# Performance work log

Measured on AMD Instinct MI355X. Metric: run time of the kernel, lower is better.

Reference implementation:

```python
import jax, jax.numpy as jnp
import numpy as np
from jax import lax

N, IC, OC, K, SDIM, H, W = 16, 512, 512, 3, 512, 32, 32
PAD, STRIDE, LR = 1, 1, 1.0
WEIGHT_SCALER = 1.0 / np.sqrt(IC * K * K) * LR   # equalized-lr conv scale
FC_SCALER = 1.0 / np.sqrt(SDIM) * LR             # equalized-lr fc scale


def setup_inputs() -> dict:
    key = jax.random.key(0)
    k1, k2, k3 = jax.random.split(key, 3)
    x = jax.random.normal(k1, (N, IC, H, W), dtype=jnp.float32)
    style = jax.random.normal(k2, (N, SDIM), dtype=jnp.float32)
    weight = jax.random.normal(k3, (OC, IC, K, K), dtype=jnp.float32)  # std = 1/lr = 1
    fc_weight = jax.random.normal(jax.random.fold_in(key, 10), (IC, SDIM), dtype=jnp.float32)
    fc_bias = jnp.zeros((IC,), dtype=jnp.float32)
    return {"x": x, "style": style, "weight": weight,
            "fc_weight": fc_weight, "fc_bias": fc_bias}


def reference(x, style, weight, fc_weight, fc_bias):
    # EqualizedFullyConnect + AddChannelwiseBias, then +1 -> modulation rates [N, iC]
    mod = jnp.einsum('ns,cs->nc', style, fc_weight) * FC_SCALER + fc_bias * LR + 1.0
    # modulated per-sample weight [N, oC, iC, kH, kW]
    w = WEIGHT_SCALER * weight[None] * mod[:, None, :, None, None]
    # demodulate: rsqrt of sum of squares over (iC, kH, kW)
    demod = lax.rsqrt(jnp.sum(w * w, axis=(2, 3, 4)) + 1e-8)  # [N, oC]
    w = w * demod[:, :, None, None, None]
    # grouped conv with groups=N == per-sample conv: vmap over batch
    def conv1(xi, wi):
        # xi: [iC,H,W], wi: [oC,iC,kH,kW]
        return lax.conv_general_dilated(
            xi[None], wi, window_strides=(STRIDE, STRIDE),
            padding=((PAD, PAD), (PAD, PAD)),
            dimension_numbers=('NCHW', 'OIHW', 'NCHW'))[0]
    out = jax.vmap(conv1)(x, w)  # [N, oC, H, W]
    return out
```

## Files before the change

kernel.cpp:

```cpp
#include <hip/hip_runtime.h>
#include <hip/hip_bf16.h>

#define N_    16
#define IC_   512
#define OC_   512
#define SDIM_ 512
#define H_    32
#define W_    32
#define HW_   1024

#define FC_SCALER 0.04419417382415922f
#define WS_       0.014731391274719738f
#define WS2_      (1.0f/4608.0f)

typedef __attribute__((__ext_vector_type__(8)))  __bf16 bf16x8;
typedef __attribute__((__ext_vector_type__(16))) float  f32x16;
typedef __attribute__((__ext_vector_type__(4)))  int    i32x4;

__device__ __forceinline__ unsigned short f2bf(float f) {
    unsigned int u = __builtin_bit_cast(unsigned int, f);
    unsigned int r = (u + 0x7FFFu + ((u >> 16) & 1u)) >> 16;
    return (unsigned short)r;
}

__global__ void k_mod(const float* __restrict__ style, const float* __restrict__ fcw,
                      const float* __restrict__ fcb, float* __restrict__ mod) {
    int gid = blockIdx.x * blockDim.x + threadIdx.x;
    int wid = gid >> 6, lane = gid & 63;
    if (wid >= N_ * IC_) return;
    int n = wid >> 9, c = wid & 511;
    const float4* sp = (const float4*)(style + n * SDIM_);
    const float4* wp = (const float4*)(fcw + (size_t)c * SDIM_);
    float acc = 0.f;
    for (int i = lane; i < SDIM_ / 4; i += 64) {
        float4 a = sp[i], b = wp[i];
        acc += a.x*b.x + a.y*b.y + a.z*b.z + a.w*b.w;
    }
#pragma unroll
    for (int off = 32; off; off >>= 1) acc += __shfl_xor(acc, off);
    if (lane == 0) mod[wid] = acc * FC_SCALER + fcb[c] + 1.0f;
}

__global__ void k_wprep(const float* __restrict__ w, unsigned short* __restrict__ wt,
                        float* __restrict__ wsq) {
    int tid = blockIdx.x * blockDim.x + threadIdx.x;
    int oc = tid >> 9, ic = tid & 511;
    float s = 0.f;
#pragma unroll
    for (int t = 0; t < 9; t++) {
        float v = w[(size_t)tid * 9 + t];
        s += v * v;
        wt[((size_t)(t * OC_ + oc)) * IC_ + ic] = f2bf(v);
    }
    wsq[tid] = s;
}

__global__ void k_demod(const float* __restrict__ mod, const float* __restrict__ wsq,
                        float* __restrict__ demod_ws) {
    int gid = blockIdx.x * blockDim.x + threadIdx.x;
    int wid = gid >> 6, lane = gid & 63;
    if (wid >= N_ * OC_) return;
    int n = wid >> 9, oc = wid & 511;
    const float4* mp = (const float4*)(mod + n * IC_);
    const float4* qp = (const float4*)(wsq + (size_t)oc * IC_);
    float acc = 0.f;
    for (int i = lane; i < IC_ / 4; i += 64) {
        float4 m = mp[i], q = qp[i];
        acc += m.x*m.x*q.x + m.y*m.y*q.y + m.z*m.z*q.z + m.w*m.w*q.w;
    }
#pragma unroll
    for (int off = 32; off; off >>= 1) acc += __shfl_xor(acc, off);
    if (lane == 0) {
        float s = WS2_ * acc + 1e-8f;
        demod_ws[wid] = WS_ / sqrtf(s);
    }
}

__global__ void k_premod(const float* __restrict__ x, const float* __restrict__ mod,
                         unsigned short* __restrict__ xm) {
    __shared__ __align__(16) unsigned short t_lds[64][80];
    int bx = blockIdx.x;
    int n = bx >> 7, hwt = (bx >> 3) & 15, ict = bx & 7;
    int hw0 = hwt * 64, ic0 = ict * 64;
    int tid = threadIdx.x, lane = tid & 63, ty = tid >> 6;
#pragma unroll
    for (int jj = 0; jj < 16; jj++) {
        int icl = ty * 16 + jj;
        float v = x[(size_t)(n * IC_ + ic0 + icl) * HW_ + hw0 + lane]
                  * mod[n * IC_ + ic0 + icl];
        t_lds[lane][icl] = f2bf(v);
    }
    __syncthreads();
#pragma unroll
    for (int rep = 0; rep < 2; rep++) {
        int hwl = rep * 32 + (tid >> 3);
        int icl8 = (tid & 7) * 8;
        i32x4 v = *(const i32x4*)&t_lds[hwl][icl8];
        *(i32x4*)(xm + ((size_t)(n * HW_ + hw0 + hwl) * IC_ + ic0 + icl8)) = v;
    }
}

#define BLK_OC 128
__global__ __launch_bounds__(256, 2)
void k_conv(const unsigned short* __restrict__ xm, const unsigned short* __restrict__ wt,
            const float* __restrict__ demod_ws, float* __restrict__ out) {
    __shared__ __align__(16) unsigned short xt[6 * 34 * 64];
    __shared__ __align__(16) unsigned short wbuf[2][128 * 64];
    __shared__ float s_demod[128];

    int bx = blockIdx.x;
    int n = bx >> 5, octile = (bx >> 3) & 3, sptile = bx & 7;
    int oc0 = octile * BLK_OC, y0 = sptile * 4;
    int tid = threadIdx.x, lane = tid & 63, wid = tid >> 6;
    int wr = wid >> 1, wc = wid & 1;

    if (tid < 128) s_demod[tid] = demod_ws[n * OC_ + oc0 + tid];

    f32x16 acc[2][2] = {};

    const unsigned short* xbase = xm + (size_t)n * HW_ * IC_;

#pragma unroll 1
    for (int icc = 0; icc < IC_ / 64; icc++) {
        int ic0 = icc * 64;
        for (int idx = tid; idx < 6 * 34 * 8; idx += 256) {
            int rc = idx >> 3, icl8 = (idx & 7) * 8;
            int rr = rc / 34, cp = rc - rr * 34;
            int yy = y0 - 1 + rr, xx = cp - 1;
            i32x4 v = {};
            if ((unsigned)yy < 32u && (unsigned)xx < 32u)
                v = *(const i32x4*)(xbase + ((size_t)(yy * W_ + xx) * IC_ + ic0 + icl8));
            int a = (rc * 128 + icl8 * 2) ^ ((rc & 7) << 4);
            *(i32x4*)((char*)xt + a) = v;
        }
        {
            const unsigned short* wsrc = wt + (size_t)oc0 * IC_ + ic0;
#pragma unroll
            for (int k = 0; k < 4; k++) {
                int c = tid + k * 256;
                int ocl = c >> 3, icl8 = (c & 7) * 8;
                i32x4 v = *(const i32x4*)(wsrc + (size_t)ocl * IC_ + icl8);
                int a = (ocl * 128 + icl8 * 2) ^ ((ocl & 7) << 4);
                *(i32x4*)((char*)wbuf[0] + a) = v;
            }
        }
        __syncthreads();

#pragma unroll
        for (int t = 0; t < 9; t++) {
            i32x4 wreg[4];
            if (t < 8) {
                const unsigned short* wsrc =
                    wt + ((size_t)((t + 1) * OC_ + oc0)) * IC_ + ic0;
#pragma unroll
                for (int k = 0; k < 4; k++) {
                    int c = tid + k * 256;
                    int ocl = c >> 3, icl8 = (c & 7) * 8;
                    wreg[k] = *(const i32x4*)(wsrc + (size_t)ocl * IC_ + icl8);
                }
            }
            int dy = t / 3, dx = t % 3;
            const unsigned short* wb = wbuf[t & 1];
#pragma unroll
            for (int kk = 0; kk < 4; kk++) {
                int koff = kk * 16 + (lane >> 5) * 8;
                bf16x8 af[2], bfr[2];
#pragma unroll
                for (int fo = 0; fo < 2; fo++) {
                    int ocl = wr * 64 + fo * 32 + (lane & 31);
                    int a = (ocl * 128 + koff * 2) ^ ((ocl & 7) << 4);
                    af[fo] = *(const bf16x8*)((const char*)wb + a);
                }
#pragma unroll
                for (int fs = 0; fs < 2; fs++) {
                    int rr = wc * 2 + fs + dy;
                    int cp = (lane & 31) + dx;
                    int rc = rr * 34 + cp;
                    int a = (rc * 128 + koff * 2) ^ ((rc & 7) << 4);
                    bfr[fs] = *(const bf16x8*)((const char*)xt + a);
                }
#pragma unroll
                for (int fo = 0; fo < 2; fo++)
#pragma unroll
                    for (int fs = 0; fs < 2; fs++)
                        acc[fo][fs] = __builtin_amdgcn_mfma_f32_32x32x16_bf16(
                            af[fo], bfr[fs], acc[fo][fs], 0, 0, 0);
            }
            if (t < 8) {
#pragma unroll
                for (int k = 0; k < 4; k++) {
                    int c = tid + k * 256;
                    int ocl = c >> 3, icl8 = (c & 7) * 8;
                    int a = (ocl * 128 + icl8 * 2) ^ ((ocl & 7) << 4);
                    *(i32x4*)((char*)wbuf[(t + 1) & 1] + a) = wreg[k];
                }
            }
            __syncthreads();
        }
    }

    int xcol = lane & 31;
#pragma unroll
    for (int fo = 0; fo < 2; fo++) {
#pragma unroll
        for (int fs = 0; fs < 2; fs++) {
            int y = y0 + wc * 2 + fs;
#pragma unroll
            for (int r = 0; r < 16; r++) {
                int row = (r & 3) + 8 * (r >> 2) + 4 * (lane >> 5);
                int ocl = wr * 64 + fo * 32 + row;
                float v = acc[fo][fs][r] * s_demod[ocl];
                out[((size_t)(n * OC_ + oc0 + ocl) * H_ + y) * W_ + xcol] = v;
            }
        }
    }
}

extern "C" void kernel_launch(void* const* d_in, const int* in_sizes, int n_in,
                              void* d_out, int out_size, void* d_ws, size_t ws_size,
                              hipStream_t stream) {
    const float* x      = (const float*)d_in[0];
    const float* style  = (const float*)d_in[1];
    const float* weight = (const float*)d_in[2];
    const float* fcw    = (const float*)d_in[3];
    const float* fcb    = (const float*)d_in[4];
    float* out = (float*)d_out;

    char* ws = (char*)d_ws;
    float*          mod   = (float*)ws;
    float*          demod = (float*)(ws + 32768);
    float*          wsq   = (float*)(ws + 65536);
    unsigned short* wtb   = (unsigned short*)(ws + 65536 + 1048576);
    unsigned short* xmb   = (unsigned short*)(ws + 65536 + 1048576 + 4718592);

    k_mod   <<<2048, 256, 0, stream>>>(style, fcw, fcb, mod);
    k_wprep <<<1024, 256, 0, stream>>>(weight, wtb, wsq);
    k_demod <<<2048, 256, 0, stream>>>(mod, wsq, demod);
    k_premod<<<2048, 256, 0, stream>>>(x, mod, xmb);
    k_conv  <<<512,  256, 0, stream>>>(xmb, wtb, demod, out);
}
```

Measured before the change: 114.6 us.

## Stage conv tiles with direct global-to-LDS loads and MFMA-friendly layouts

```diff
diff --git a/kernel.cpp b/kernel.cpp
--- a/kernel.cpp
+++ b/kernel.cpp
@@ -16,6 +16,9 @@
 typedef __attribute__((__ext_vector_type__(8)))  __bf16 bf16x8;
 typedef __attribute__((__ext_vector_type__(16))) float  f32x16;
 typedef __attribute__((__ext_vector_type__(4)))  int    i32x4;
+
+typedef __attribute__((address_space(1))) const unsigned int GInt;
+typedef __attribute__((address_space(3))) unsigned int LInt;
 
 __device__ __forceinline__ unsigned short f2bf(float f) {
     unsigned int u = __builtin_bit_cast(unsigned int, f);
@@ -45,12 +48,16 @@
                         float* __restrict__ wsq) {
     int tid = blockIdx.x * blockDim.x + threadIdx.x;
     int oc = tid >> 9, ic = tid & 511;
+    int og = oc >> 7, ocl = oc & 127;
+    int icc = ic >> 6, k6 = ic & 63, ks = k6 >> 3, i8 = k6 & 7;
     float s = 0.f;
 #pragma unroll
     for (int t = 0; t < 9; t++) {
         float v = w[(size_t)tid * 9 + t];
         s += v * v;
-        wt[((size_t)(t * OC_ + oc)) * IC_ + ic] = f2bf(v);
+        size_t off = ((((size_t)t * 4 + og) * 8 + icc) * 8192)
+                   + (size_t)ks * 1024 + ocl * 8 + i8;
+        wt[off] = f2bf(v);
     }
     wsq[tid] = s;
 }
@@ -91,126 +98,125 @@
         t_lds[lane][icl] = f2bf(v);
     }
     __syncthreads();
+    int xcol = tid & 31, ks = tid >> 5;
 #pragma unroll
     for (int rep = 0; rep < 2; rep++) {
-        int hwl = rep * 32 + (tid >> 3);
-        int icl8 = (tid & 7) * 8;
-        i32x4 v = *(const i32x4*)&t_lds[hwl][icl8];
-        *(i32x4*)(xm + ((size_t)(n * HW_ + hw0 + hwl) * IC_ + ic0 + icl8)) = v;
-    }
-}
-
-#define BLK_OC 128
-__global__ __launch_bounds__(256, 2)
+        int hwl = rep * 32 + xcol;
+        i32x4 v = *(const i32x4*)&t_lds[hwl][ks * 8];
+        int y = (hw0 >> 5) + rep;
+        size_t off = ((((size_t)n * 8 + ict) * 32 + y) * 8 + ks) * 256 + xcol * 8;
+        *(i32x4*)(xm + off) = v;
+    }
+}
+
+__global__ __launch_bounds__(256, 1)
 void k_conv(const unsigned short* __restrict__ xm, const unsigned short* __restrict__ wt,
             const float* __restrict__ demod_ws, float* __restrict__ out) {
-    __shared__ __align__(16) unsigned short xt[6 * 34 * 64];
-    __shared__ __align__(16) unsigned short wbuf[2][128 * 64];
+    __shared__ __align__(16) unsigned short xt[2][10 * 2048];
+    __shared__ __align__(16) unsigned short wb[2][8192];
+    __shared__ __align__(16) float zslot[4];
     __shared__ float s_demod[128];
 
     int bx = blockIdx.x;
-    int n = bx >> 5, octile = (bx >> 3) & 3, sptile = bx & 7;
-    int oc0 = octile * BLK_OC, y0 = sptile * 4;
+    int octg = bx >> 6, n = (bx >> 2) & 15, spt = bx & 3;
+    int oc0 = octg * 128, y0 = spt * 8;
     int tid = threadIdx.x, lane = tid & 63, wid = tid >> 6;
-    int wr = wid >> 1, wc = wid & 1;
+    int l31 = lane & 31, lhi = lane >> 5;
 
     if (tid < 128) s_demod[tid] = demod_ws[n * OC_ + oc0 + tid];
-
-    f32x16 acc[2][2] = {};
-
-    const unsigned short* xbase = xm + (size_t)n * HW_ * IC_;
-
+    if (tid == 0) { zslot[0] = 0.f; zslot[1] = 0.f; zslot[2] = 0.f; zslot[3] = 0.f; }
+    if (spt == 0) {
+        i32x4 z = {};
+        *(i32x4*)&xt[0][tid * 8] = z;
+        *(i32x4*)&xt[1][tid * 8] = z;
+    }
+    if (spt == 3) {
+        i32x4 z = {};
+        *(i32x4*)&xt[0][9 * 2048 + tid * 8] = z;
+        *(i32x4*)&xt[1][9 * 2048 + tid * 8] = z;
+    }
+
+    const unsigned short* xsrc_n = xm + (size_t)n * (8 * 32 * 2048);
+
+    auto stage_x = [&](int buf, int icc) {
+        for (int wl = wid; wl < 40; wl += 4) {
+            int rr = wl >> 2, j = wl & 3;
+            int y = y0 - 1 + rr;
+            if ((unsigned)y < 32u) {
+                const unsigned short* g =
+                    xsrc_n + ((size_t)icc * 32 + y) * 2048 + j * 512 + lane * 8;
+                unsigned short* l = &xt[buf][rr * 2048 + j * 512];
+                __builtin_amdgcn_global_load_lds((GInt*)g, (LInt*)l, 16, 0, 0);
+            }
+        }
+    };
+    auto stage_w = [&](int buf, int tap, int icc) {
+        const unsigned short* wsrcc = wt + (((size_t)tap * 4 + octg) * 8 + icc) * 8192;
+        for (int wl = wid; wl < 16; wl += 4) {
+            const unsigned short* g = wsrcc + wl * 512 + lane * 8;
+            unsigned short* l = &wb[buf][wl * 512];
+            __builtin_amdgcn_global_load_lds((GInt*)g, (LInt*)l, 16, 0, 0);
+        }
+    };
+
+    f32x16 acc[4][2] = {};
+
+    stage_x(0, 0);
+    stage_w(0, 0, 0);
+    __syncthreads();
+
+    int xb = 0, wcur = 0;
 #pragma unroll 1
-    for (int icc = 0; icc < IC_ / 64; icc++) {
-        int ic0 = icc * 64;
-        for (int idx = tid; idx < 6 * 34 * 8; idx += 256) {
-            int rc = idx >> 3, icl8 = (idx & 7) * 8;
-            int rr = rc / 34, cp = rc - rr * 34;
-            int yy = y0 - 1 + rr, xx = cp - 1;
-            i32x4 v = {};
-            if ((unsigned)yy < 32u && (unsigned)xx < 32u)
-                v = *(const i32x4*)(xbase + ((size_t)(yy * W_ + xx) * IC_ + ic0 + icl8));
-            int a = (rc * 128 + icl8 * 2) ^ ((rc & 7) << 4);
-            *(i32x4*)((char*)xt + a) = v;
-        }
-        {
-            const unsigned short* wsrc = wt + (size_t)oc0 * IC_ + ic0;
-#pragma unroll
-            for (int k = 0; k < 4; k++) {
-                int c = tid + k * 256;
-                int ocl = c >> 3, icl8 = (c & 7) * 8;
-                i32x4 v = *(const i32x4*)(wsrc + (size_t)ocl * IC_ + icl8);
-                int a = (ocl * 128 + icl8 * 2) ^ ((ocl & 7) << 4);
-                *(i32x4*)((char*)wbuf[0] + a) = v;
-            }
-        }
-        __syncthreads();
-
-#pragma unroll
+    for (int icc = 0; icc < 8; icc++) {
+#pragma unroll 1
         for (int t = 0; t < 9; t++) {
-            i32x4 wreg[4];
-            if (t < 8) {
-                const unsigned short* wsrc =
-                    wt + ((size_t)((t + 1) * OC_ + oc0)) * IC_ + ic0;
-#pragma unroll
-                for (int k = 0; k < 4; k++) {
-                    int c = tid + k * 256;
-                    int ocl = c >> 3, icl8 = (c & 7) * 8;
-                    wreg[k] = *(const i32x4*)(wsrc + (size_t)ocl * IC_ + icl8);
+            if (t == 0 && icc < 7) stage_x(xb ^ 1, icc + 1);
+            if (t < 8)              stage_w(wcur ^ 1, t + 1, icc);
+            else if (icc < 7)       stage_w(wcur ^ 1, 0, icc + 1);
+
+            int dy = t / 3, dx = t % 3;
+            const unsigned short* wbp = wb[wcur];
+            const unsigned short* xtp = xt[xb];
+#pragma unroll
+            for (int kk = 0; kk < 4; kk++) {
+                int kslot = kk * 2 + lhi;
+                bf16x8 af[4], bfr[2];
+#pragma unroll
+                for (int fo = 0; fo < 4; fo++)
+                    af[fo] = *(const bf16x8*)(wbp + kslot * 1024 + (fo * 32 + l31) * 8);
+#pragma unroll
+                for (int fs = 0; fs < 2; fs++) {
+                    int rr = wid * 2 + fs + dy;
+                    unsigned cp = (unsigned)(l31 + dx) - 1u;
+                    const unsigned short* p = (cp < 32u)
+                        ? (xtp + rr * 2048 + kslot * 256 + cp * 8)
+                        : (const unsigned short*)zslot;
+                    bfr[fs] = *(const bf16x8*)p;
                 }
-            }
-            int dy = t / 3, dx = t % 3;
-            const unsigned short* wb = wbuf[t & 1];
-#pragma unroll
-            for (int kk = 0; kk < 4; kk++) {
-                int koff = kk * 16 + (lane >> 5) * 8;
-                bf16x8 af[2], bfr[2];
-#pragma unroll
-                for (int fo = 0; fo < 2; fo++) {
-                    int ocl = wr * 64 + fo * 32 + (lane & 31);
-                    int a = (ocl * 128 + koff * 2) ^ ((ocl & 7) << 4);
-                    af[fo] = *(const bf16x8*)((const char*)wb + a);
-                }
-#pragma unroll
-                for (int fs = 0; fs < 2; fs++) {
-                    int rr = wc * 2 + fs + dy;
-                    int cp = (lane & 31) + dx;
-                    int rc = rr * 34 + cp;
-                    int a = (rc * 128 + koff * 2) ^ ((rc & 7) << 4);
-                    bfr[fs] = *(const bf16x8*)((const char*)xt + a);
-                }
-#pragma unroll
-                for (int fo = 0; fo < 2; fo++)
+#pragma unroll
+                for (int fo = 0; fo < 4; fo++)
 #pragma unroll
                     for (int fs = 0; fs < 2; fs++)
                         acc[fo][fs] = __builtin_amdgcn_mfma_f32_32x32x16_bf16(
                             af[fo], bfr[fs], acc[fo][fs], 0, 0, 0);
             }
-            if (t < 8) {
-#pragma unroll
-                for (int k = 0; k < 4; k++) {
-                    int c = tid + k * 256;
-                    int ocl = c >> 3, icl8 = (c & 7) * 8;
-                    int a = (ocl * 128 + icl8 * 2) ^ ((ocl & 7) << 4);
-                    *(i32x4*)((char*)wbuf[(t + 1) & 1] + a) = wreg[k];
-                }
-            }
             __syncthreads();
-        }
-    }
-
-    int xcol = lane & 31;
-#pragma unroll
-    for (int fo = 0; fo < 2; fo++) {
+            wcur ^= 1;
+        }
+        xb ^= 1;
+    }
+
+#pragma unroll
+    for (int fo = 0; fo < 4; fo++) {
 #pragma unroll
         for (int fs = 0; fs < 2; fs++) {
-            int y = y0 + wc * 2 + fs;
+            int y = y0 + wid * 2 + fs;
 #pragma unroll
             for (int r = 0; r < 16; r++) {
-                int row = (r & 3) + 8 * (r >> 2) + 4 * (lane >> 5);
-                int ocl = wr * 64 + fo * 32 + row;
+                int row = (r & 3) + 8 * (r >> 2) + 4 * lhi;
+                int ocl = fo * 32 + row;
                 float v = acc[fo][fs][r] * s_demod[ocl];
-                out[((size_t)(n * OC_ + oc0 + ocl) * H_ + y) * W_ + xcol] = v;
+                out[((size_t)(n * OC_ + oc0 + ocl) * H_ + y) * W_ + l31] = v;
             }
         }
     }
@@ -237,5 +243,5 @@
     k_wprep <<<1024, 256, 0, stream>>>(weight, wtb, wsq);
     k_demod <<<2048, 256, 0, stream>>>(mod, wsq, demod);
     k_premod<<<2048, 256, 0, stream>>>(x, mod, xmb);
-    k_conv  <<<512,  256, 0, stream>>>(xmb, wtb, demod, out);
-}
+    k_conv  <<<256,  256, 0, stream>>>(xmb, wtb, demod, out);
+}
```

New measurement: 118.3 us. +3.3%, slower.
